# Performance work log

Hardware: AMD Instinct MI355X
Metric: run time of the kernel (lower is better)

Reference implementation:

```python
import jax, jax.numpy as jnp
import numpy as np

K_CONST = 1.0  # margin constant K from __init__


def setup_inputs() -> dict:
    key = jax.random.key(0)
    k1, k2, k3 = jax.random.split(key, 3)
    m, n, d = 2048, 100000, 128
    return {
        "X_tilde": jax.random.normal(k1, (m, d), dtype=jnp.float32),
        "X": jax.random.normal(k2, (n, d), dtype=jnp.float32),
        "w": jax.random.normal(k3, (n, 1), dtype=jnp.float32),
        "k": 10,
    }


def reference(X_tilde, X, w, k):
    # w_prime = sqrt((max(w) - w) / K), appended as extra coordinate for the
    # augmented exact L2 search (queries padded with 0 in that coordinate).
    w_prime2 = (jnp.max(w) - w)[:, 0] / K_CONST  # (n,) == w_prime**2
    # squared L2 in augmented space: ||q||^2 + ||x||^2 + w_prime^2 - 2 q.x
    q2 = jnp.sum(X_tilde * X_tilde, axis=1, keepdims=True)           # (m,1)
    x2 = jnp.sum(X * X, axis=1) + w_prime2                            # (n,)
    d2 = q2 + x2[None, :] - 2.0 * (X_tilde @ X.T)                     # (m,n)
    _, idx = jax.lax.top_k(-d2, k)                                    # (m,k) nearest
    # gather neighbors and recompute actual (non-augmented) L2 distance
    nb = X[idx]                                                       # (m,k,d)
    diff = nb - X_tilde[:, None, :]
    dist = jnp.sqrt(jnp.sum(diff * diff, axis=2))                     # (m,k)
    act = w[idx, 0] - K_CONST * dist                                  # (m,k)
    # argmax + gather == max over the k neighbors
    return jnp.max(act, axis=1)                                       # (m,)
```

## Files before the change

### kernel.cpp

```cpp
#include <hip/hip_runtime.h>
#include <math.h>

typedef __attribute__((ext_vector_type(8))) short short8;
typedef __attribute__((ext_vector_type(16))) float f32x16;

#define D      128
#define NSEG   128
#define NHSEG  256
#define SEGC   800
#define NT     25
#define TPP    5
#define NPART  5
#define TILE_C 32
#define KTOP   10
#define CAP    128
#define DELTA  3.0f
#define NPAD   (NSEG * SEGC + TILE_C)
#define ROWU   128
#define TUNITS (TILE_C * 16)
#define BUFU   (TUNITS * 8)
#define MQ     2048
#define WQCAP  (NSEG * 8 * NPART)

__device__ __forceinline__ int swz16(int u) {
    int r = u >> 4, kb = u & 15;
    return r * 16 + (kb ^ (r & 7));
}

__device__ __forceinline__ ushort f2bf(float f) {
    uint u = __float_as_uint(f);
    uint r = (u + 0x7FFFu + ((u >> 16) & 1u)) >> 16;
    return (ushort)r;
}

__device__ __forceinline__ uint packx2(float x2w) {
    ushort h = f2bf(x2w);
    float hf = __uint_as_float(((uint)h) << 16);
    ushort lo = f2bf(x2w - hf);
    return (uint)h | ((uint)lo << 16);
}

__device__ __forceinline__ void insert10(float s, float v, float ls[KTOP], float lw[KTOP]) {
    ls[9] = s; lw[9] = v;
#pragma unroll
    for (int p = 9; p > 0; --p) {
        bool sw = ls[p] < ls[p - 1];
        float ts = sw ? ls[p - 1] : ls[p];
        float tl = sw ? ls[p]     : ls[p - 1];
        float tv = sw ? lw[p - 1] : lw[p];
        float tu = sw ? lw[p]     : lw[p - 1];
        ls[p] = ts; ls[p - 1] = tl;
        lw[p] = tv; lw[p - 1] = tu;
    }
}

__device__ __forceinline__ void insert10s(float s, float ms[KTOP]) {
    ms[9] = s;
#pragma unroll
    for (int p = 9; p > 0; --p) {
        float a = fminf(ms[p - 1], ms[p]);
        float b = fmaxf(ms[p - 1], ms[p]);
        ms[p - 1] = a; ms[p] = b;
    }
}

__global__ void prep_kernel(const float* __restrict__ Xt, const float* __restrict__ X,
                            const float* __restrict__ w,
                            ushort* __restrict__ Xbp, ushort* __restrict__ Xtb,
                            uint* __restrict__ x2wp,
                            float* __restrict__ x2wf, float* __restrict__ q2f,
                            int* __restrict__ cnt, int* __restrict__ wq_n,
                            int n, int m, int nblocksA) {
    if (blockIdx.x == 0 && threadIdx.x == 0) wq_n[0] = 0;
    int wave = threadIdx.x >> 6, lane = threadIdx.x & 63;
    if ((int)blockIdx.x < nblocksA) {
        int row = blockIdx.x * 4 + wave;
        if (row >= NPAD) return;
        ushort* rowp = Xbp + (size_t)row * ROWU;
        if (row < n) {
            float2 v = ((const float2*)X)[(size_t)row * 64 + lane];
            ((ushort2*)rowp)[lane] = make_ushort2(f2bf(v.x), f2bf(v.y));
            float s = v.x * v.x + v.y * v.y;
#pragma unroll
            for (int o = 32; o; o >>= 1) s += __shfl_xor(s, o, 64);
            float x2w = s - w[row];
            if (lane == 0) { x2wf[row] = x2w; x2wp[row] = packx2(x2w); }
        } else {
            ((ushort2*)rowp)[lane] = make_ushort2(0, 0);
            if (lane == 0) x2wp[row] = packx2(1e30f);
        }
    } else {
        int qb = blockIdx.x - nblocksA;
        int row = qb * 4 + wave;
        int tid = qb * 256 + threadIdx.x;
        if (tid < m) cnt[tid] = 0;
        if (row >= m) return;
        float2 v = ((const float2*)Xt)[(size_t)row * 64 + lane];
        ((ushort2*)Xtb)[(size_t)row * 64 + lane] = make_ushort2(f2bf(v.x), f2bf(v.y));
        float s = v.x * v.x + v.y * v.y;
#pragma unroll
        for (int o = 32; o; o >>= 1) s += __shfl_xor(s, o, 64);
        if (lane == 0) q2f[row] = s;
    }
}

__device__ __forceinline__ void emit_cand(int q, int c, int* cnt, int* buf) {
    int pos = atomicAdd(&cnt[q], 1);
    if (pos < CAP) buf[q * CAP + pos] = c;
}

__global__ __launch_bounds__(256, 4) void nd_pass1(
        const ushort* __restrict__ Xbp, const ushort* __restrict__ Xtb,
        const uint* __restrict__ x2wp,
        float* __restrict__ minbuf, int m) {
    __shared__ __align__(16) ushort As[2 * BUFU];

    const int t = threadIdx.x;
    const int l = t & 63, wv = t >> 6;
    const int half = l >> 5;
    const int hs = blockIdx.x;
    const int seg = hs >> 1, sub = hs & 1;
    const int tile0 = seg * NT + sub * 13;
    const int ntile = 13 - sub;
    const int qbase = blockIdx.y * 256 + wv * 64;
    const int q0 = qbase + (l & 31);

    short8 Bf[8][2];
#pragma unroll
    for (int s = 0; s < 8; ++s)
#pragma unroll
        for (int qs = 0; qs < 2; ++qs)
            Bf[s][qs] = *(const short8*)(Xtb + (size_t)(q0 + qs * 32) * D + s * 16 + half * 8);
    short8 B8 = (short8)(short)0;
    if (l < 32) { B8[0] = (short)0xBF00; B8[1] = (short)0xBF00; }

    float mx0 = -INFINITY, mx1 = -INFINITY;

    const int u0 = t, u1 = 256 + t;
    const int L0 = swz16(u0) * 8, L1 = swz16(u1) * 8;
    const uint4* Xg = (const uint4*)Xbp;
    int raddr[8];
#pragma unroll
    for (int ks = 0; ks < 8; ++ks)
        raddr[ks] = ((l & 31) * 16 + ((2 * ks + half) ^ (l & 7))) * 8;

    uint4 r0 = Xg[(size_t)tile0 * TUNITS + u0];
    uint4 r1 = Xg[(size_t)tile0 * TUNITS + u1];
    uint pkc = x2wp[tile0 * TILE_C + (l & 31)];

    for (int t2 = 0; t2 < ntile; ++t2) {
        ushort* Lb = &As[(t2 & 1) * BUFU];
        *(uint4*)&Lb[L0] = r0;
        *(uint4*)&Lb[L1] = r1;
        __syncthreads();

        const size_t gb = (size_t)(tile0 + t2 + 1) * TUNITS;
        r0 = Xg[gb + u0];
        r1 = Xg[gb + u1];
        uint pkn = x2wp[(tile0 + t2 + 1) * TILE_C + (l & 31)];

        f32x16 acc0 = (f32x16)0.f, acc1 = (f32x16)0.f;
#pragma unroll
        for (int ks = 0; ks < 8; ++ks) {
            short8 a = *(const short8*)&Lb[raddr[ks]];
            acc0 = __builtin_amdgcn_mfma_f32_32x32x16_bf16(a, Bf[ks][0], acc0, 0, 0, 0);
            acc1 = __builtin_amdgcn_mfma_f32_32x32x16_bf16(a, Bf[ks][1], acc1, 0, 0, 0);
        }
        short8 av9 = (short8)(short)0;
        av9[0] = (short)(pkc & 0xffff);
        av9[1] = (short)(pkc >> 16);
        acc0 = __builtin_amdgcn_mfma_f32_32x32x16_bf16(av9, B8, acc0, 0, 0, 0);
        acc1 = __builtin_amdgcn_mfma_f32_32x32x16_bf16(av9, B8, acc1, 0, 0, 0);
        pkc = pkn;

        float h0 = -INFINITY, h1 = -INFINITY;
#pragma unroll
        for (int r = 0; r < 16; ++r) { h0 = fmaxf(h0, acc0[r]); h1 = fmaxf(h1, acc1[r]); }
        mx0 = fmaxf(mx0, h0);
        mx1 = fmaxf(mx1, h1);
    }

    size_t rowi = (size_t)(hs * 2 + half) * m;
    minbuf[rowi + q0]      = -2.f * mx0;
    minbuf[rowi + q0 + 32] = -2.f * mx1;
}

__global__ void tau_kernel(const float* __restrict__ minbuf, float* __restrict__ tau, int m) {
    __shared__ float sh[64 * 40];
    const int qi = threadIdx.x & 63, part = threadIdx.x >> 6;
    const int q = blockIdx.x * 64 + qi;
    float ms[KTOP];
#pragma unroll
    for (int e = 0; e < KTOP; ++e) ms[e] = INFINITY;
#pragma unroll 4
    for (int i = 0; i < 128; ++i) {
        float v = minbuf[(size_t)(part * 128 + i) * m + q];
        if (v < ms[9]) insert10s(v, ms);
    }
#pragma unroll
    for (int e = 0; e < KTOP; ++e) sh[qi * 40 + part * 10 + e] = ms[e];
    __syncthreads();
    if (threadIdx.x < 64) {
        const int qq = blockIdx.x * 64 + threadIdx.x;
        float fs[KTOP];
#pragma unroll
        for (int e = 0; e < KTOP; ++e) fs[e] = INFINITY;
        for (int x = 0; x < 40; ++x) {
            float v = sh[threadIdx.x * 40 + x];
            if (v < fs[9]) insert10s(v, fs);
        }
        tau[qq] = fs[9] + DELTA;
    }
}

__global__ void list_build(const float* __restrict__ minbuf, const float* __restrict__ tau,
                           int* __restrict__ qlist, int* __restrict__ wq,
                           int* __restrict__ wq_n, int m) {
    __shared__ int lq[MQ];
    __shared__ int lcnt;
    const int s = blockIdx.x, tid = threadIdx.x;
    if (tid == 0) lcnt = 0;
    __syncthreads();
    const float* r0 = minbuf + (size_t)(4 * s) * m;
    const float* r1 = minbuf + (size_t)(4 * s + 1) * m;
    const float* r2 = minbuf + (size_t)(4 * s + 2) * m;
    const float* r3 = minbuf + (size_t)(4 * s + 3) * m;
    for (int q = tid; q < m; q += 256) {
        float v = fminf(fminf(r0[q], r1[q]), fminf(r2[q], r3[q]));
        if (v <= tau[q]) { int p = atomicAdd(&lcnt, 1); lq[p] = q; }
    }
    __syncthreads();
    const int c = lcnt;
    const int padded = (c + 255) & ~255;
    for (int i = c + tid; i < padded; i += 256) lq[i] = -1;
    __syncthreads();
    for (int i = tid; i < padded; i += 256) qlist[(size_t)s * MQ + i] = lq[i];
    if (tid == 0 && c > 0) {
        const int nqc = padded >> 8;
        int base = atomicAdd(wq_n, nqc * NPART);
        for (int qc = 0; qc < nqc; ++qc)
            for (int p = 0; p < NPART; ++p)
                wq[base++] = (s << 6) | (qc << 3) | p;
    }
}

__global__ __launch_bounds__(256, 4) void nd_pass2(
        const ushort* __restrict__ Xbp, const ushort* __restrict__ Xtb,
        const uint* __restrict__ x2wp, const float* __restrict__ tau,
        int* __restrict__ cnt, int* __restrict__ buf,
        const int* __restrict__ qlist, const int* __restrict__ wq,
        const int* __restrict__ wq_n, int m) {
    __shared__ __align__(16) ushort As[2 * BUFU];

    const int t = threadIdx.x;
    const int l = t & 63, wv = t >> 6;
    const int half = l >> 5;
    const int u0 = t, u1 = 256 + t;
    const int L0 = swz16(u0) * 8, L1 = swz16(u1) * 8;
    const uint4* Xg = (const uint4*)Xbp;
    int raddr[8];
#pragma unroll
    for (int ks = 0; ks < 8; ++ks)
        raddr[ks] = ((l & 31) * 16 + ((2 * ks + half) ^ (l & 7))) * 8;
    const int T = wq_n[0];

    for (int w = blockIdx.x; w < T; w += gridDim.x) {
        const int it = wq[w];
        const int s = it >> 6, qc = (it >> 3) & 7, part = it & 7;
        const int t0 = s * NT + part * TPP;
        const int lbase = s * MQ + qc * 256 + wv * 64 + (l & 31);
        const int qi0 = qlist[lbase], qi1 = qlist[lbase + 32];
        const int q0e = qi0 < 0 ? 0 : qi0, q1e = qi1 < 0 ? 0 : qi1;

        short8 Bf[8][2];
#pragma unroll
        for (int sk = 0; sk < 8; ++sk) {
            Bf[sk][0] = *(const short8*)(Xtb + (size_t)q0e * D + sk * 16 + half * 8);
            Bf[sk][1] = *(const short8*)(Xtb + (size_t)q1e * D + sk * 16 + half * 8);
        }
        short8 B8 = (short8)(short)0;
        if (l < 32) { B8[0] = (short)0xBF00; B8[1] = (short)0xBF00; }
        const float tp0 = (qi0 < 0) ? INFINITY : (-0.5f * tau[qi0]);
        const float tp1 = (qi1 < 0) ? INFINITY : (-0.5f * tau[qi1]);

        uint4 r0 = Xg[(size_t)t0 * TUNITS + u0];
        uint4 r1 = Xg[(size_t)t0 * TUNITS + u1];
        uint pkc = x2wp[t0 * TILE_C + (l & 31)];

        for (int t2 = t0; t2 < t0 + TPP; ++t2) {
            ushort* Lb = &As[(t2 & 1) * BUFU];
            *(uint4*)&Lb[L0] = r0;
            *(uint4*)&Lb[L1] = r1;
            __syncthreads();

            const size_t gb = (size_t)(t2 + 1) * TUNITS;
            r0 = Xg[gb + u0];
            r1 = Xg[gb + u1];
            uint pkn = x2wp[(t2 + 1) * TILE_C + (l & 31)];

            f32x16 acc0 = (f32x16)0.f, acc1 = (f32x16)0.f;
#pragma unroll
            for (int ks = 0; ks < 8; ++ks) {
                short8 a = *(const short8*)&Lb[raddr[ks]];
                acc0 = __builtin_amdgcn_mfma_f32_32x32x16_bf16(a, Bf[ks][0], acc0, 0, 0, 0);
                acc1 = __builtin_amdgcn_mfma_f32_32x32x16_bf16(a, Bf[ks][1], acc1, 0, 0, 0);
            }
            short8 av9 = (short8)(short)0;
            av9[0] = (short)(pkc & 0xffff);
            av9[1] = (short)(pkc >> 16);
            acc0 = __builtin_amdgcn_mfma_f32_32x32x16_bf16(av9, B8, acc0, 0, 0, 0);
            acc1 = __builtin_amdgcn_mfma_f32_32x32x16_bf16(av9, B8, acc1, 0, 0, 0);
            pkc = pkn;

            float h0 = -INFINITY, h1 = -INFINITY;
#pragma unroll
            for (int r = 0; r < 16; ++r) { h0 = fmaxf(h0, acc0[r]); h1 = fmaxf(h1, acc1[r]); }
            const int base = t2 * TILE_C;
            if (__any(h0 >= tp0)) {
#pragma unroll
                for (int r = 0; r < 16; ++r)
                    if (acc0[r] >= tp0) emit_cand(qi0, base + (r & 3) + 8 * (r >> 2) + 4 * half, cnt, buf);
            }
            if (__any(h1 >= tp1)) {
#pragma unroll
                for (int r = 0; r < 16; ++r)
                    if (acc1[r] >= tp1) emit_cand(qi1, base + (r & 3) + 8 * (r >> 2) + 4 * half, cnt, buf);
            }
        }
        __syncthreads();
    }
}

__global__ void rescore_kernel(const float* __restrict__ Xtf, const float* __restrict__ Xf,
                               const float* __restrict__ w, const float* __restrict__ x2wf,
                               const float* __restrict__ q2f, const int* __restrict__ cnt,
                               const int* __restrict__ buf, float* __restrict__ out, int m) {
    __shared__ float sS[CAP], sW[CAP];
    const int q = blockIdx.x, l = threadIdx.x;
    const int c = min(cnt[q], CAP);
    const bool v0 = l < c, v1 = l + 64 < c;
    const int j0 = v0 ? buf[q * CAP + l] : 0;
    const int j1 = v1 ? buf[q * CAP + l + 64] : 0;
    const float4* Q4 = (const float4*)Xtf + (size_t)q * 32;
    const float4* A4 = (const float4*)Xf + (size_t)j0 * 32;
    const float4* B4 = (const float4*)Xf + (size_t)j1 * 32;
    float acc0 = 0.f, acc1 = 0.f;
#pragma unroll 8
    for (int d = 0; d < 32; ++d) {
        float4 qv = Q4[d];
        float4 a = A4[d], b = B4[d];
        acc0 = fmaf(qv.x, a.x, fmaf(qv.y, a.y, fmaf(qv.z, a.z, fmaf(qv.w, a.w, acc0))));
        acc1 = fmaf(qv.x, b.x, fmaf(qv.y, b.y, fmaf(qv.z, b.z, fmaf(qv.w, b.w, acc1))));
    }
    sS[l]      = v0 ? (x2wf[j0] - 2.f * acc0) : INFINITY;
    sW[l]      = v0 ? w[j0] : 0.f;
    sS[l + 64] = v1 ? (x2wf[j1] - 2.f * acc1) : INFINITY;
    sW[l + 64] = v1 ? w[j1] : 0.f;
    __syncthreads();
    if (l == 0) {
        float ls[KTOP], lw[KTOP];
#pragma unroll
        for (int e = 0; e < KTOP; ++e) { ls[e] = INFINITY; lw[e] = 0.f; }
        for (int i = 0; i < c; ++i)
            if (sS[i] < ls[9]) insert10(sS[i], sW[i], ls, lw);
        float q2v = q2f[q];
        float mxv = -INFINITY;
#pragma unroll
        for (int e = 0; e < KTOP; ++e) {
            if (ls[e] < 1e30f) {
                float d2 = fmaxf(q2v + ls[e] + lw[e], 0.f);
                mxv = fmaxf(mxv, lw[e] - sqrtf(d2));
            }
        }
        out[q] = mxv;
    }
}

extern "C" void kernel_launch(void* const* d_in, const int* in_sizes, int n_in,
                              void* d_out, int out_size, void* d_ws, size_t ws_size,
                              hipStream_t stream) {
    const float* Xt = (const float*)d_in[0];
    const float* X  = (const float*)d_in[1];
    const float* w  = (const float*)d_in[2];
    const int m = in_sizes[0] / D;
    const int n = in_sizes[1] / D;

    auto align256 = [](size_t x) { return (x + 255) & ~(size_t)255; };
    char* p = (char*)d_ws;
    ushort* Xbp  = (ushort*)p;  p += align256((size_t)NPAD * ROWU * 2);
    ushort* Xtb  = (ushort*)p;  p += align256((size_t)m * D * 2);
    uint*   x2wp = (uint*)p;    p += align256((size_t)NPAD * 4);
    float*  x2wf = (float*)p;   p += align256((size_t)n * 4);
    float*  q2f  = (float*)p;   p += align256((size_t)m * 4);
    float*  minb = (float*)p;   p += align256((size_t)4 * NSEG * m * 4);
    float*  tau  = (float*)p;   p += align256((size_t)m * 4);
    int*    cnt  = (int*)p;     p += align256((size_t)m * 4);
    int*    buf  = (int*)p;     p += align256((size_t)m * CAP * 4);
    int*    qlist= (int*)p;     p += align256((size_t)NSEG * MQ * 4);
    int*    wq   = (int*)p;     p += align256((size_t)WQCAP * 4);
    int*    wq_n = (int*)p;     p += align256((size_t)256);

    const int nblocksA = (NPAD + 3) / 4;
    const int nblocksB = (m + 3) / 4;
    prep_kernel<<<nblocksA + nblocksB, 256, 0, stream>>>(Xt, X, w, Xbp, Xtb, x2wp, x2wf, q2f,
                                                         cnt, wq_n, n, m, nblocksA);

    dim3 grid1(NHSEG, m / 256);
    nd_pass1<<<grid1, 256, 0, stream>>>(Xbp, Xtb, x2wp, minb, m);
    tau_kernel<<<m / 64, 256, 0, stream>>>(minb, tau, m);
    list_build<<<NSEG, 256, 0, stream>>>(minb, tau, qlist, wq, wq_n, m);
    nd_pass2<<<1024, 256, 0, stream>>>(Xbp, Xtb, x2wp, tau, cnt, buf, qlist, wq, wq_n, m);
    rescore_kernel<<<m, 64, 0, stream>>>(Xt, X, w, x2wf, q2f, cnt, buf, (float*)d_out, m);
}
```

Before: 270.0 us.

## Load pass-1 tiles directly into LDS with async global_load_lds, two-tile stages

Replaces the register-staged global-to-LDS copy in the first-pass distance kernel with global_load_lds direct-to-LDS loads. The LDS buffer grows to four tiles so two tiles are processed per barrier while the next pair streams in. The swizzle moves from the LDS write to the global source address. The goal is to cut VGPR staging, store instructions and barrier count, at the cost of doubled LDS use (which may limit occupancy), extra padding reads past the end, and an odd-tile tail path.

```diff
diff --git a/kernel.cpp b/kernel.cpp
--- a/kernel.cpp
+++ b/kernel.cpp
@@ -15,7 +15,7 @@
 #define KTOP   10
 #define CAP    128
 #define DELTA  3.0f
-#define NPAD   (NSEG * SEGC + TILE_C)
+#define NPAD   (NSEG * SEGC + 2 * TILE_C)
 #define ROWU   128
 #define TUNITS (TILE_C * 16)
 #define BUFU   (TUNITS * 8)
@@ -25,6 +25,12 @@
 __device__ __forceinline__ int swz16(int u) {
     int r = u >> 4, kb = u & 15;
     return r * 16 + (kb ^ (r & 7));
+}
+
+__device__ __forceinline__ void gl_lds16(const ushort* g, ushort* lds) {
+    __builtin_amdgcn_global_load_lds(
+        (const __attribute__((address_space(1))) unsigned int*)g,
+        (__attribute__((address_space(3))) unsigned int*)lds, 16, 0, 0);
 }
 
 __device__ __forceinline__ ushort f2bf(float f) {
@@ -109,11 +115,38 @@
     if (pos < CAP) buf[q * CAP + pos] = c;
 }
 
+#define STAGE1(T, buf) do {                                                          \
+    const ushort* gA_ = Xbp + ((size_t)(T) * TUNITS + g0u) * 8;                      \
+    const ushort* gB_ = Xbp + ((size_t)(T) * TUNITS + g1u) * 8;                      \
+    gl_lds16(gA_, &As[(size_t)(buf) * BUFU + (size_t)(wv * 128) * 8]);               \
+    gl_lds16(gB_, &As[(size_t)(buf) * BUFU + (size_t)(wv * 128 + 64) * 8]);          \
+} while (0)
+
+#define CTILE1(buf, pk) do {                                                         \
+    const char* Lc_ = (const char*)&As[(size_t)(buf) * BUFU];                        \
+    f32x16 acc0 = (f32x16)0.f, acc1 = (f32x16)0.f;                                   \
+    _Pragma("unroll")                                                                \
+    for (int ks = 0; ks < 8; ++ks) {                                                 \
+        short8 a = *(const short8*)(Lc_ + rbase + ((ks << 5) ^ hx16));               \
+        acc0 = __builtin_amdgcn_mfma_f32_32x32x16_bf16(a, Bf[ks][0], acc0, 0, 0, 0); \
+        acc1 = __builtin_amdgcn_mfma_f32_32x32x16_bf16(a, Bf[ks][1], acc1, 0, 0, 0); \
+    }                                                                                \
+    short8 av9 = (short8)(short)0;                                                   \
+    av9[0] = (short)((pk) & 0xffff);                                                 \
+    av9[1] = (short)((pk) >> 16);                                                    \
+    acc0 = __builtin_amdgcn_mfma_f32_32x32x16_bf16(av9, B8, acc0, 0, 0, 0);          \
+    acc1 = __builtin_amdgcn_mfma_f32_32x32x16_bf16(av9, B8, acc1, 0, 0, 0);          \
+    float h0 = -INFINITY, h1 = -INFINITY;                                            \
+    _Pragma("unroll")                                                                \
+    for (int r = 0; r < 16; ++r) { h0 = fmaxf(h0, acc0[r]); h1 = fmaxf(h1, acc1[r]); } \
+    mx0 = fmaxf(mx0, h0); mx1 = fmaxf(mx1, h1);                                      \
+} while (0)
+
 __global__ __launch_bounds__(256, 4) void nd_pass1(
         const ushort* __restrict__ Xbp, const ushort* __restrict__ Xtb,
         const uint* __restrict__ x2wp,
         float* __restrict__ minbuf, int m) {
-    __shared__ __align__(16) ushort As[2 * BUFU];
+    __shared__ __align__(16) ushort As[4 * BUFU];
 
     const int t = threadIdx.x;
     const int l = t & 63, wv = t >> 6;
@@ -136,54 +169,39 @@
 
     float mx0 = -INFINITY, mx1 = -INFINITY;
 
-    const int u0 = t, u1 = 256 + t;
-    const int L0 = swz16(u0) * 8, L1 = swz16(u1) * 8;
-    const uint4* Xg = (const uint4*)Xbp;
-    int raddr[8];
-#pragma unroll
-    for (int ks = 0; ks < 8; ++ks)
-        raddr[ks] = ((l & 31) * 16 + ((2 * ks + half) ^ (l & 7))) * 8;
-
-    uint4 r0 = Xg[(size_t)tile0 * TUNITS + u0];
-    uint4 r1 = Xg[(size_t)tile0 * TUNITS + u1];
-    uint pkc = x2wp[tile0 * TILE_C + (l & 31)];
-
-    for (int t2 = 0; t2 < ntile; ++t2) {
-        ushort* Lb = &As[(t2 & 1) * BUFU];
-        *(uint4*)&Lb[L0] = r0;
-        *(uint4*)&Lb[L1] = r1;
+    const int g0u = swz16(wv * 128 + l);
+    const int g1u = swz16(wv * 128 + 64 + l);
+    const int rbase = (l & 31) * 256;
+    const int hx16 = (half ^ (l & 7)) << 4;
+
+    STAGE1(tile0 + 0, 0);
+    STAGE1(tile0 + 1, 1);
+    __syncthreads();
+
+    const int nr = ntile >> 1;
+    for (int r2 = 0; r2 < nr; ++r2) {
+        const int pair = (r2 & 1) * 2;
+        const int npair = 2 - pair;
+        const int tn = tile0 + 2 * r2;
+        STAGE1(tn + 2, npair + 0);
+        STAGE1(tn + 3, npair + 1);
+        const uint pka = x2wp[tn * TILE_C + (l & 31)];
+        const uint pkb = x2wp[(tn + 1) * TILE_C + (l & 31)];
+        CTILE1(pair + 0, pka);
+        CTILE1(pair + 1, pkb);
         __syncthreads();
-
-        const size_t gb = (size_t)(tile0 + t2 + 1) * TUNITS;
-        r0 = Xg[gb + u0];
-        r1 = Xg[gb + u1];
-        uint pkn = x2wp[(tile0 + t2 + 1) * TILE_C + (l & 31)];
-
-        f32x16 acc0 = (f32x16)0.f, acc1 = (f32x16)0.f;
-#pragma unroll
-        for (int ks = 0; ks < 8; ++ks) {
-            short8 a = *(const short8*)&Lb[raddr[ks]];
-            acc0 = __builtin_amdgcn_mfma_f32_32x32x16_bf16(a, Bf[ks][0], acc0, 0, 0, 0);
-            acc1 = __builtin_amdgcn_mfma_f32_32x32x16_bf16(a, Bf[ks][1], acc1, 0, 0, 0);
-        }
-        short8 av9 = (short8)(short)0;
-        av9[0] = (short)(pkc & 0xffff);
-        av9[1] = (short)(pkc >> 16);
-        acc0 = __builtin_amdgcn_mfma_f32_32x32x16_bf16(av9, B8, acc0, 0, 0, 0);
-        acc1 = __builtin_amdgcn_mfma_f32_32x32x16_bf16(av9, B8, acc1, 0, 0, 0);
-        pkc = pkn;
-
-        float h0 = -INFINITY, h1 = -INFINITY;
-#pragma unroll
-        for (int r = 0; r < 16; ++r) { h0 = fmaxf(h0, acc0[r]); h1 = fmaxf(h1, acc1[r]); }
-        mx0 = fmaxf(mx0, h0);
-        mx1 = fmaxf(mx1, h1);
+    }
+    if (ntile & 1) {
+        const uint pka = x2wp[(tile0 + 2 * nr) * TILE_C + (l & 31)];
+        CTILE1((nr & 1) * 2, pka);
     }
 
     size_t rowi = (size_t)(hs * 2 + half) * m;
     minbuf[rowi + q0]      = -2.f * mx0;
     minbuf[rowi + q0 + 32] = -2.f * mx1;
 }
+#undef STAGE1
+#undef CTILE1
 
 __global__ void tau_kernel(const float* __restrict__ minbuf, float* __restrict__ tau, int m) {
     __shared__ float sh[64 * 40];
```

New measurement: 319.0 us. 1.18x slower.
